# Performance work log

Measured on AMD Instinct MI355X. Metric: run time of the kernel, lower is better.

## Reference

```python
import jax, jax.numpy as jnp
import numpy as np

MAX_LANES = 5
DELTA_V = 1.0
DELTA_D = 6.0


def setup_inputs() -> dict:
    key = jax.random.key(0)
    k1, k2 = jax.random.split(key)
    targets = jax.random.randint(k1, (32, 360, 640), 0, 6, dtype=jnp.int32)
    embedding_vector = jax.random.normal(k2, (32, 4, 360, 640), dtype=jnp.float32)
    return {"targets": targets, "embedding_vector": embedding_vector}


def reference(targets, embedding_vector):
    B, C, H, W = embedding_vector.shape
    L = MAX_LANES
    P = H * W
    t = targets.reshape(B, P)                      # [B,P] labels 0..L
    e = embedding_vector.reshape(B, C, P)          # [B,C,P]

    # per-(batch, lane) segment counts and means
    onehot = (t[:, None, :] == jnp.arange(1, L + 1, dtype=t.dtype)[None, :, None])  # [B,L,P]
    counts = onehot.sum(-1)                        # [B,L] int
    valid = counts > 1                             # lane used only if >1 points
    sums = jnp.einsum('blp,bcp->blc', onehot.astype(e.dtype), e)   # [B,L,C]
    means = sums / jnp.maximum(counts, 1)[..., None].astype(e.dtype)  # [B,L,C]

    # ---- variance (pull) loss: per-point distance to its lane mean ----
    means_ext = jnp.concatenate([jnp.zeros((B, 1, C), e.dtype), means], axis=1)  # [B,L+1,C]
    mean_pix = jnp.take_along_axis(means_ext, t[..., None].astype(jnp.int32), axis=1)  # [B,P,C]
    diff = e.transpose(0, 2, 1) - mean_pix         # [B,P,C]
    sq = jnp.sum(diff * diff, axis=-1)             # [B,P]
    dist = jnp.sqrt(jnp.maximum(sq, 1e-12))
    valid_ext = jnp.concatenate([jnp.zeros((B, 1), bool), valid], axis=1)  # [B,L+1]
    pix_valid = jnp.take_along_axis(valid_ext, t.astype(jnp.int32), axis=1)  # [B,P]
    hinge = jax.nn.relu(dist - DELTA_V)
    dist_sum = jnp.sum(jnp.where(pix_valid, hinge * hinge, 0.0))
    point_count = jnp.sum(jnp.where(valid, counts, 0)).astype(e.dtype)
    dist_loss = jnp.where(point_count > 0, dist_sum / jnp.maximum(point_count, 1.0), 0.0)

    # ---- distance (push) loss: pdist over valid lane means per batch ----
    d = means[:, :, None, :] - means[:, None, :, :]          # [B,L,L,C]
    psq = jnp.sum(d * d, axis=-1)                            # [B,L,L]
    pd = jnp.sqrt(jnp.maximum(psq, 1e-12))
    iu = jnp.arange(L)
    pair_mask = valid[:, :, None] & valid[:, None, :] & (iu[:, None] < iu[None, :])  # [B,L,L]
    ph = jax.nn.relu(DELTA_D - pd)
    per_batch_sum = jnp.sum(jnp.where(pair_mask, ph * ph, 0.0), axis=(1, 2))  # [B]
    npairs = pair_mask.sum((1, 2)).astype(e.dtype)           # [B]
    batch_has = npairs > 0                                   # needs >=2 valid lanes
    var_b = jnp.where(batch_has, per_batch_sum / jnp.maximum(npairs, 1.0), 0.0)
    n_batches = batch_has.sum().astype(e.dtype)
    var_loss = jnp.where(n_batches > 0, var_b.sum() / jnp.maximum(n_batches, 1.0), 0.0)

    return dist_loss + var_loss
```

## Files before the change

### kernel.cpp

```cpp
#include <hip/hip_runtime.h>
#include <math.h>

#define B 32
#define C 4
#define H 360
#define W 640
#define P (H*W)
#define L 5
#define DELTA_V 1.0f
#define DELTA_D 6.0f

#define NV 25
#define BLK1 32
#define NBLK (B*BLK1)
#define G4 (P/4)

__device__ __forceinline__ float waveReduce(float v) {
#pragma unroll
    for (int off = 32; off; off >>= 1) v += __shfl_down(v, off, 64);
    return v;
}

__global__ __launch_bounds__(256) void seg_sums_k(const int* __restrict__ tgt,
                                                  const float* __restrict__ emb,
                                                  float* __restrict__ part1) {
    const int b = blockIdx.y;
    float s[L][C];
    float cn[L];
#pragma unroll
    for (int l = 0; l < L; ++l) {
        cn[l] = 0.f;
#pragma unroll
        for (int c = 0; c < C; ++c) s[l][c] = 0.f;
    }

    const int4*   t4 = (const int4*)(tgt + (size_t)b * P);
    const float4* e0 = (const float4*)(emb + (size_t)(b*C + 0) * P);
    const float4* e1 = (const float4*)(emb + (size_t)(b*C + 1) * P);
    const float4* e2 = (const float4*)(emb + (size_t)(b*C + 2) * P);
    const float4* e3 = (const float4*)(emb + (size_t)(b*C + 3) * P);

    auto proc = [&](int tt, float x0, float x1, float x2, float x3) {
#pragma unroll
        for (int l = 0; l < L; ++l) {
            float m = (tt == l + 1) ? 1.0f : 0.0f;
            cn[l] += m;
            s[l][0] = fmaf(m, x0, s[l][0]);
            s[l][1] = fmaf(m, x1, s[l][1]);
            s[l][2] = fmaf(m, x2, s[l][2]);
            s[l][3] = fmaf(m, x3, s[l][3]);
        }
    };

    for (int g = blockIdx.x * 256 + threadIdx.x; g < G4; g += BLK1 * 256) {
        int4   t  = t4[g];
        float4 a0 = e0[g], a1 = e1[g], a2 = e2[g], a3 = e3[g];
        proc(t.x, a0.x, a1.x, a2.x, a3.x);
        proc(t.y, a0.y, a1.y, a2.y, a3.y);
        proc(t.z, a0.z, a1.z, a2.z, a3.z);
        proc(t.w, a0.w, a1.w, a2.w, a3.w);
    }

    float vals[NV];
#pragma unroll
    for (int l = 0; l < L; ++l) {
#pragma unroll
        for (int c = 0; c < C; ++c) vals[l*4 + c] = s[l][c];
        vals[20 + l] = cn[l];
    }

    __shared__ float red[4][NV];
    const int lane = threadIdx.x & 63, wave = threadIdx.x >> 6;
#pragma unroll
    for (int k = 0; k < NV; ++k) {
        float r = waveReduce(vals[k]);
        if (lane == 0) red[wave][k] = r;
    }
    __syncthreads();
    if (threadIdx.x < NV) {
        float r = red[0][threadIdx.x] + red[1][threadIdx.x]
                + red[2][threadIdx.x] + red[3][threadIdx.x];
        part1[(size_t)(b * BLK1 + blockIdx.x) * NV + threadIdx.x] = r;
    }
}

__global__ __launch_bounds__(256) void finalize_k(const float* __restrict__ part1,
                                                  float* __restrict__ means,
                                                  float* __restrict__ validf,
                                                  float* __restrict__ misc) {
    __shared__ float smean[B*L*C];
    __shared__ float svalid[B*L];
    __shared__ float lred[4];
    const int tid = threadIdx.x;
    const int lane = tid & 63, wave = tid >> 6;

    float pc = 0.f;
    if (tid < B*L) {
        const int b = tid / L, l = tid % L;
        float sm[C] = {0.f, 0.f, 0.f, 0.f};
        float cnt = 0.f;
        for (int blk = 0; blk < BLK1; ++blk) {
            const float* p = part1 + (size_t)(b * BLK1 + blk) * NV;
#pragma unroll
            for (int c = 0; c < C; ++c) sm[c] += p[l*4 + c];
            cnt += p[20 + l];
        }
        const float inv = 1.0f / fmaxf(cnt, 1.0f);
        const bool  v   = cnt > 1.5f;
#pragma unroll
        for (int c = 0; c < C; ++c) {
            float m = sm[c] * inv;
            smean[tid*C + c] = m;
            means[tid*C + c] = m;
        }
        svalid[tid] = v ? 1.f : 0.f;
        validf[tid] = v ? 1.f : 0.f;
        if (v) pc = cnt;
    }

    {
        float r = waveReduce(pc);
        if (lane == 0) lred[wave] = r;
    }
    __syncthreads();
    if (tid == 0) misc[1] = lred[0] + lred[1] + lred[2] + lred[3];

    float vb = 0.f, has = 0.f;
    if (tid < B) {
        const int base = tid * L;
        float ssum = 0.f, np = 0.f;
#pragma unroll
        for (int i = 0; i < L; ++i) {
#pragma unroll
            for (int j = i + 1; j < L; ++j) {
                float ok = svalid[base+i] * svalid[base+j];
                float d0 = smean[(base+i)*C+0] - smean[(base+j)*C+0];
                float d1 = smean[(base+i)*C+1] - smean[(base+j)*C+1];
                float d2 = smean[(base+i)*C+2] - smean[(base+j)*C+2];
                float d3 = smean[(base+i)*C+3] - smean[(base+j)*C+3];
                float psq = d0*d0 + d1*d1 + d2*d2 + d3*d3;
                float pd  = sqrtf(fmaxf(psq, 1e-12f));
                float ph  = fmaxf(DELTA_D - pd, 0.f);
                ssum += ok * ph * ph;
                np   += ok;
            }
        }
        if (np > 0.f) { vb = ssum / np; has = 1.f; }
    }
    if (wave == 0) {
        float vr = waveReduce(vb);
        float hr = waveReduce(has);
        if (tid == 0) misc[0] = (hr > 0.f) ? vr / hr : 0.f;
    }
}

__global__ __launch_bounds__(256) void pull_k(const int* __restrict__ tgt,
                                              const float* __restrict__ emb,
                                              const float* __restrict__ means,
                                              const float* __restrict__ validf,
                                              float* __restrict__ part3) {
    __shared__ float4 lmean[L + 1];
    __shared__ float  lvalid[L + 1];
    __shared__ float  lred[4];
    const int b = blockIdx.y;
    const int tid = threadIdx.x;

    if (tid == 0) { lmean[0] = make_float4(0.f, 0.f, 0.f, 0.f); lvalid[0] = 0.f; }
    else if (tid <= L) {
        lmean[tid]  = *(const float4*)(means + ((size_t)b*L + (tid-1)) * C);
        lvalid[tid] = validf[b*L + (tid-1)];
    }
    __syncthreads();

    const int4*   t4 = (const int4*)(tgt + (size_t)b * P);
    const float4* e0 = (const float4*)(emb + (size_t)(b*C + 0) * P);
    const float4* e1 = (const float4*)(emb + (size_t)(b*C + 1) * P);
    const float4* e2 = (const float4*)(emb + (size_t)(b*C + 2) * P);
    const float4* e3 = (const float4*)(emb + (size_t)(b*C + 3) * P);

    float acc = 0.f;
    auto proc = [&](int tt, float x0, float x1, float x2, float x3) {
        float4 m = lmean[tt];
        float d0 = x0 - m.x, d1 = x1 - m.y, d2 = x2 - m.z, d3 = x3 - m.w;
        float sq   = d0*d0 + d1*d1 + d2*d2 + d3*d3;
        float dist = sqrtf(fmaxf(sq, 1e-12f));
        float h    = fmaxf(dist - DELTA_V, 0.f);
        acc = fmaf(lvalid[tt] * h, h, acc);
    };

    for (int g = blockIdx.x * 256 + threadIdx.x; g < G4; g += BLK1 * 256) {
        int4   t  = t4[g];
        float4 a0 = e0[g], a1 = e1[g], a2 = e2[g], a3 = e3[g];
        proc(t.x, a0.x, a1.x, a2.x, a3.x);
        proc(t.y, a0.y, a1.y, a2.y, a3.y);
        proc(t.z, a0.z, a1.z, a2.z, a3.z);
        proc(t.w, a0.w, a1.w, a2.w, a3.w);
    }

    float r = waveReduce(acc);
    const int lane = tid & 63, wave = tid >> 6;
    if (lane == 0) lred[wave] = r;
    __syncthreads();
    if (tid == 0)
        part3[b * BLK1 + blockIdx.x] = lred[0] + lred[1] + lred[2] + lred[3];
}

__global__ __launch_bounds__(256) void finish_k(const float* __restrict__ part3,
                                                const float* __restrict__ misc,
                                                float* __restrict__ out) {
    __shared__ float lred[4];
    const int tid = threadIdx.x;
    float s = 0.f;
    for (int i = tid; i < NBLK; i += 256) s += part3[i];
    float r = waveReduce(s);
    const int lane = tid & 63, wave = tid >> 6;
    if (lane == 0) lred[wave] = r;
    __syncthreads();
    if (tid == 0) {
        float ds  = lred[0] + lred[1] + lred[2] + lred[3];
        float pcv = misc[1];
        float dl  = (pcv > 0.f) ? ds / fmaxf(pcv, 1.0f) : 0.f;
        out[0] = dl + misc[0];
    }
}

extern "C" void kernel_launch(void* const* d_in, const int* in_sizes, int n_in,
                              void* d_out, int out_size, void* d_ws, size_t ws_size,
                              hipStream_t stream) {
    const int*   tgt = (const int*)d_in[0];
    const float* emb = (const float*)d_in[1];

    float* ws     = (float*)d_ws;
    float* part1  = ws;
    float* means  = part1 + (size_t)NBLK * NV;
    float* validf = means + B*L*C;
    float* misc   = validf + B*L;
    float* part3  = misc + 4;

    dim3 grid(BLK1, B);
    seg_sums_k<<<grid, 256, 0, stream>>>(tgt, emb, part1);
    finalize_k<<<1, 256, 0, stream>>>(part1, means, validf, misc);
    pull_k<<<grid, 256, 0, stream>>>(tgt, emb, means, validf, part3);
    finish_k<<<1, 256, 0, stream>>>(part3, misc, (float*)d_out);
}
```

Baseline: 227.4 us.

## Fuse all four loss kernels into one cooperative persistent kernel with grid syncs

Replaces the four launches with a single cooperative kernel that computes segment sums, lane means, the pull loss and the final reduction, separated by grid-wide syncs. Work is split into 2048 fixed tiles spread over a persistent grid sized from occupancy, and the inner loop is unrolled two float4 groups per iteration. The means finalisation is now spread across blocks instead of running on a single block. This removes launch gaps and the serial single-block finalize, at the cost of grid-sync overhead and a hardcoded 256-CU grid assumption.

```diff
diff --git a/kernel.cpp b/kernel.cpp
--- a/kernel.cpp
+++ b/kernel.cpp
@@ -1,19 +1,20 @@
 #include <hip/hip_runtime.h>
+#include <hip/hip_cooperative_groups.h>
 #include <math.h>
 
+namespace cg = cooperative_groups;
+
 #define B 32
-#define C 4
-#define H 360
-#define W 640
-#define P (H*W)
+#define P (360*640)
 #define L 5
 #define DELTA_V 1.0f
 #define DELTA_D 6.0f
 
-#define NV 25
-#define BLK1 32
-#define NBLK (B*BLK1)
 #define G4 (P/4)
+#define CHUNKS 64
+#define NT (B*CHUNKS)
+#define CG 900
+#define NVP 32
 
 __device__ __forceinline__ float waveReduce(float v) {
 #pragma unroll
@@ -21,206 +22,197 @@
     return v;
 }
 
-__global__ __launch_bounds__(256) void seg_sums_k(const int* __restrict__ tgt,
+__global__ __launch_bounds__(256, 4) void fused_k(const int* __restrict__ tgt,
                                                   const float* __restrict__ emb,
-                                                  float* __restrict__ part1) {
-    const int b = blockIdx.y;
-    float s[L][C];
-    float cn[L];
-#pragma unroll
-    for (int l = 0; l < L; ++l) {
-        cn[l] = 0.f;
-#pragma unroll
-        for (int c = 0; c < C; ++c) s[l][c] = 0.f;
-    }
-
-    const int4*   t4 = (const int4*)(tgt + (size_t)b * P);
-    const float4* e0 = (const float4*)(emb + (size_t)(b*C + 0) * P);
-    const float4* e1 = (const float4*)(emb + (size_t)(b*C + 1) * P);
-    const float4* e2 = (const float4*)(emb + (size_t)(b*C + 2) * P);
-    const float4* e3 = (const float4*)(emb + (size_t)(b*C + 3) * P);
-
-    auto proc = [&](int tt, float x0, float x1, float x2, float x3) {
+                                                  float* ws, float* out) {
+    cg::grid_group gg = cg::this_grid();
+    const int tid  = threadIdx.x;
+    const int lane = tid & 63, wave = tid >> 6;
+    const int nb   = gridDim.x;
+
+    float* part   = ws;
+    float* means  = part + (size_t)NT*NVP;
+    float* validf = means + B*L*4;
+    float* cntv   = validf + B*L;
+    float* pullp  = cntv + B*L;
+
+    __shared__ float  red[4][32];
+    __shared__ float4 lmean[8];
+    __shared__ float  lvalid[8];
+
+    for (int tile = blockIdx.x; tile < NT; tile += nb) {
+        const int b  = tile >> 6;
+        const int gs = (tile & 63) * CG, ge = gs + CG;
+        const int4*   t4 = (const int4*)(tgt + (size_t)b * P);
+        const float4* e0 = (const float4*)(emb + (size_t)(b*4+0) * P);
+        const float4* e1 = (const float4*)(emb + (size_t)(b*4+1) * P);
+        const float4* e2 = (const float4*)(emb + (size_t)(b*4+2) * P);
+        const float4* e3 = (const float4*)(emb + (size_t)(b*4+3) * P);
+
+        float s[L][4], cn[L];
+#pragma unroll
+        for (int l = 0; l < L; ++l) { cn[l]=0.f; s[l][0]=s[l][1]=s[l][2]=s[l][3]=0.f; }
+
+        auto proc = [&](int tt, float x0, float x1, float x2, float x3) {
+#pragma unroll
+            for (int l = 0; l < L; ++l) {
+                float m = (tt == l+1) ? 1.f : 0.f;
+                cn[l] += m;
+                s[l][0] = fmaf(m, x0, s[l][0]);
+                s[l][1] = fmaf(m, x1, s[l][1]);
+                s[l][2] = fmaf(m, x2, s[l][2]);
+                s[l][3] = fmaf(m, x3, s[l][3]);
+            }
+        };
+
+        for (int g0 = gs + tid; g0 < ge; g0 += 512) {
+            const int g1  = g0 + 256;
+            const int gg1 = (g1 < ge) ? g1 : g0;
+            int4   t0v = t4[g0],  t1v = t4[gg1];
+            float4 a00 = e0[g0],  a01 = e1[g0],  a02 = e2[g0],  a03 = e3[g0];
+            float4 a10 = e0[gg1], a11 = e1[gg1], a12 = e2[gg1], a13 = e3[gg1];
+            if (g1 >= ge) { t1v.x = 0; t1v.y = 0; t1v.z = 0; t1v.w = 0; }
+            proc(t0v.x, a00.x, a01.x, a02.x, a03.x);
+            proc(t0v.y, a00.y, a01.y, a02.y, a03.y);
+            proc(t0v.z, a00.z, a01.z, a02.z, a03.z);
+            proc(t0v.w, a00.w, a01.w, a02.w, a03.w);
+            proc(t1v.x, a10.x, a11.x, a12.x, a13.x);
+            proc(t1v.y, a10.y, a11.y, a12.y, a13.y);
+            proc(t1v.z, a10.z, a11.z, a12.z, a13.z);
+            proc(t1v.w, a10.w, a11.w, a12.w, a13.w);
+        }
+
+        float vals[25];
 #pragma unroll
         for (int l = 0; l < L; ++l) {
-            float m = (tt == l + 1) ? 1.0f : 0.0f;
-            cn[l] += m;
-            s[l][0] = fmaf(m, x0, s[l][0]);
-            s[l][1] = fmaf(m, x1, s[l][1]);
-            s[l][2] = fmaf(m, x2, s[l][2]);
-            s[l][3] = fmaf(m, x3, s[l][3]);
-        }
-    };
-
-    for (int g = blockIdx.x * 256 + threadIdx.x; g < G4; g += BLK1 * 256) {
-        int4   t  = t4[g];
-        float4 a0 = e0[g], a1 = e1[g], a2 = e2[g], a3 = e3[g];
-        proc(t.x, a0.x, a1.x, a2.x, a3.x);
-        proc(t.y, a0.y, a1.y, a2.y, a3.y);
-        proc(t.z, a0.z, a1.z, a2.z, a3.z);
-        proc(t.w, a0.w, a1.w, a2.w, a3.w);
-    }
-
-    float vals[NV];
-#pragma unroll
-    for (int l = 0; l < L; ++l) {
-#pragma unroll
-        for (int c = 0; c < C; ++c) vals[l*4 + c] = s[l][c];
-        vals[20 + l] = cn[l];
-    }
-
-    __shared__ float red[4][NV];
-    const int lane = threadIdx.x & 63, wave = threadIdx.x >> 6;
-#pragma unroll
-    for (int k = 0; k < NV; ++k) {
-        float r = waveReduce(vals[k]);
-        if (lane == 0) red[wave][k] = r;
-    }
-    __syncthreads();
-    if (threadIdx.x < NV) {
-        float r = red[0][threadIdx.x] + red[1][threadIdx.x]
-                + red[2][threadIdx.x] + red[3][threadIdx.x];
-        part1[(size_t)(b * BLK1 + blockIdx.x) * NV + threadIdx.x] = r;
-    }
-}
-
-__global__ __launch_bounds__(256) void finalize_k(const float* __restrict__ part1,
-                                                  float* __restrict__ means,
-                                                  float* __restrict__ validf,
-                                                  float* __restrict__ misc) {
-    __shared__ float smean[B*L*C];
-    __shared__ float svalid[B*L];
-    __shared__ float lred[4];
-    const int tid = threadIdx.x;
-    const int lane = tid & 63, wave = tid >> 6;
-
-    float pc = 0.f;
-    if (tid < B*L) {
-        const int b = tid / L, l = tid % L;
-        float sm[C] = {0.f, 0.f, 0.f, 0.f};
-        float cnt = 0.f;
-        for (int blk = 0; blk < BLK1; ++blk) {
-            const float* p = part1 + (size_t)(b * BLK1 + blk) * NV;
-#pragma unroll
-            for (int c = 0; c < C; ++c) sm[c] += p[l*4 + c];
-            cnt += p[20 + l];
-        }
-        const float inv = 1.0f / fmaxf(cnt, 1.0f);
-        const bool  v   = cnt > 1.5f;
-#pragma unroll
-        for (int c = 0; c < C; ++c) {
-            float m = sm[c] * inv;
-            smean[tid*C + c] = m;
-            means[tid*C + c] = m;
-        }
-        svalid[tid] = v ? 1.f : 0.f;
-        validf[tid] = v ? 1.f : 0.f;
-        if (v) pc = cnt;
-    }
-
-    {
-        float r = waveReduce(pc);
-        if (lane == 0) lred[wave] = r;
-    }
-    __syncthreads();
-    if (tid == 0) misc[1] = lred[0] + lred[1] + lred[2] + lred[3];
+            vals[l*4+0]=s[l][0]; vals[l*4+1]=s[l][1];
+            vals[l*4+2]=s[l][2]; vals[l*4+3]=s[l][3];
+            vals[20+l]=cn[l];
+        }
+#pragma unroll
+        for (int k = 0; k < 25; ++k) {
+            float r = waveReduce(vals[k]);
+            if (lane == 0) red[wave][k] = r;
+        }
+        __syncthreads();
+        if (tid < 25)
+            part[(size_t)tile*NVP + tid] = red[0][tid]+red[1][tid]+red[2][tid]+red[3][tid];
+        __syncthreads();
+    }
+    gg.sync();
+
+    for (int sg = blockIdx.x; sg < B*L; sg += nb) {
+        if (tid < 64) {
+            const int bb = sg / L, l = sg % L;
+            const float* pp = part + (size_t)(bb*CHUNKS + tid) * NVP;
+            float v0=pp[l*4+0], v1=pp[l*4+1], v2=pp[l*4+2], v3=pp[l*4+3], vc=pp[20+l];
+            v0=waveReduce(v0); v1=waveReduce(v1); v2=waveReduce(v2);
+            v3=waveReduce(v3); vc=waveReduce(vc);
+            if (lane == 0) {
+                const float inv = 1.f / fmaxf(vc, 1.f);
+                const bool  vl  = vc > 1.5f;
+                means[sg*4+0]=v0*inv; means[sg*4+1]=v1*inv;
+                means[sg*4+2]=v2*inv; means[sg*4+3]=v3*inv;
+                validf[sg] = vl ? 1.f : 0.f;
+                cntv[sg]   = vl ? vc  : 0.f;
+            }
+        }
+    }
+    gg.sync();
+
+    for (int tile = blockIdx.x; tile < NT; tile += nb) {
+        const int b  = tile >> 6;
+        const int gs = (tile & 63) * CG, ge = gs + CG;
+        __syncthreads();
+        if (tid == 0) { lmean[0] = make_float4(0.f,0.f,0.f,0.f); lvalid[0] = 0.f; }
+        else if (tid <= L) {
+            lmean[tid]  = *(const float4*)(means + ((size_t)b*L + tid-1)*4);
+            lvalid[tid] = validf[b*L + tid-1];
+        }
+        __syncthreads();
+
+        const int4*   t4 = (const int4*)(tgt + (size_t)b * P);
+        const float4* e0 = (const float4*)(emb + (size_t)(b*4+0) * P);
+        const float4* e1 = (const float4*)(emb + (size_t)(b*4+1) * P);
+        const float4* e2 = (const float4*)(emb + (size_t)(b*4+2) * P);
+        const float4* e3 = (const float4*)(emb + (size_t)(b*4+3) * P);
+
+        float acc = 0.f;
+        auto proc3 = [&](int tt, float x0, float x1, float x2, float x3) {
+            float4 m = lmean[tt];
+            float d0 = x0-m.x, d1 = x1-m.y, d2 = x2-m.z, d3 = x3-m.w;
+            float sq   = d0*d0 + d1*d1 + d2*d2 + d3*d3;
+            float dist = sqrtf(fmaxf(sq, 1e-12f));
+            float h    = fmaxf(dist - DELTA_V, 0.f);
+            acc = fmaf(lvalid[tt]*h, h, acc);
+        };
+
+        for (int g0 = gs + tid; g0 < ge; g0 += 512) {
+            const int g1  = g0 + 256;
+            const int gg1 = (g1 < ge) ? g1 : g0;
+            int4   t0v = t4[g0],  t1v = t4[gg1];
+            float4 a00 = e0[g0],  a01 = e1[g0],  a02 = e2[g0],  a03 = e3[g0];
+            float4 a10 = e0[gg1], a11 = e1[gg1], a12 = e2[gg1], a13 = e3[gg1];
+            if (g1 >= ge) { t1v.x = 0; t1v.y = 0; t1v.z = 0; t1v.w = 0; }
+            proc3(t0v.x, a00.x, a01.x, a02.x, a03.x);
+            proc3(t0v.y, a00.y, a01.y, a02.y, a03.y);
+            proc3(t0v.z, a00.z, a01.z, a02.z, a03.z);
+            proc3(t0v.w, a00.w, a01.w, a02.w, a03.w);
+            proc3(t1v.x, a10.x, a11.x, a12.x, a13.x);
+            proc3(t1v.y, a10.y, a11.y, a12.y, a13.y);
+            proc3(t1v.z, a10.z, a11.z, a12.z, a13.z);
+            proc3(t1v.w, a10.w, a11.w, a12.w, a13.w);
+        }
+
+        float r = waveReduce(acc);
+        if (lane == 0) red[wave][0] = r;
+        __syncthreads();
+        if (tid == 0) pullp[tile] = red[0][0]+red[1][0]+red[2][0]+red[3][0];
+    }
+    gg.sync();
+
+    if (blockIdx.x != 0) return;
 
     float vb = 0.f, has = 0.f;
     if (tid < B) {
-        const int base = tid * L;
+        const float* mb = means  + tid*L*4;
+        const float* vv = validf + tid*L;
         float ssum = 0.f, np = 0.f;
 #pragma unroll
-        for (int i = 0; i < L; ++i) {
-#pragma unroll
-            for (int j = i + 1; j < L; ++j) {
-                float ok = svalid[base+i] * svalid[base+j];
-                float d0 = smean[(base+i)*C+0] - smean[(base+j)*C+0];
-                float d1 = smean[(base+i)*C+1] - smean[(base+j)*C+1];
-                float d2 = smean[(base+i)*C+2] - smean[(base+j)*C+2];
-                float d3 = smean[(base+i)*C+3] - smean[(base+j)*C+3];
+        for (int i = 0; i < L; ++i)
+#pragma unroll
+            for (int j = i+1; j < L; ++j) {
+                float ok = vv[i]*vv[j];
+                float d0 = mb[i*4+0]-mb[j*4+0];
+                float d1 = mb[i*4+1]-mb[j*4+1];
+                float d2 = mb[i*4+2]-mb[j*4+2];
+                float d3 = mb[i*4+3]-mb[j*4+3];
                 float psq = d0*d0 + d1*d1 + d2*d2 + d3*d3;
                 float pd  = sqrtf(fmaxf(psq, 1e-12f));
                 float ph  = fmaxf(DELTA_D - pd, 0.f);
-                ssum += ok * ph * ph;
+                ssum += ok*ph*ph;
                 np   += ok;
             }
-        }
-        if (np > 0.f) { vb = ssum / np; has = 1.f; }
-    }
-    if (wave == 0) {
-        float vr = waveReduce(vb);
-        float hr = waveReduce(has);
-        if (tid == 0) misc[0] = (hr > 0.f) ? vr / hr : 0.f;
-    }
-}
-
-__global__ __launch_bounds__(256) void pull_k(const int* __restrict__ tgt,
-                                              const float* __restrict__ emb,
-                                              const float* __restrict__ means,
-                                              const float* __restrict__ validf,
-                                              float* __restrict__ part3) {
-    __shared__ float4 lmean[L + 1];
-    __shared__ float  lvalid[L + 1];
-    __shared__ float  lred[4];
-    const int b = blockIdx.y;
-    const int tid = threadIdx.x;
-
-    if (tid == 0) { lmean[0] = make_float4(0.f, 0.f, 0.f, 0.f); lvalid[0] = 0.f; }
-    else if (tid <= L) {
-        lmean[tid]  = *(const float4*)(means + ((size_t)b*L + (tid-1)) * C);
-        lvalid[tid] = validf[b*L + (tid-1)];
-    }
-    __syncthreads();
-
-    const int4*   t4 = (const int4*)(tgt + (size_t)b * P);
-    const float4* e0 = (const float4*)(emb + (size_t)(b*C + 0) * P);
-    const float4* e1 = (const float4*)(emb + (size_t)(b*C + 1) * P);
-    const float4* e2 = (const float4*)(emb + (size_t)(b*C + 2) * P);
-    const float4* e3 = (const float4*)(emb + (size_t)(b*C + 3) * P);
-
-    float acc = 0.f;
-    auto proc = [&](int tt, float x0, float x1, float x2, float x3) {
-        float4 m = lmean[tt];
-        float d0 = x0 - m.x, d1 = x1 - m.y, d2 = x2 - m.z, d3 = x3 - m.w;
-        float sq   = d0*d0 + d1*d1 + d2*d2 + d3*d3;
-        float dist = sqrtf(fmaxf(sq, 1e-12f));
-        float h    = fmaxf(dist - DELTA_V, 0.f);
-        acc = fmaf(lvalid[tt] * h, h, acc);
-    };
-
-    for (int g = blockIdx.x * 256 + threadIdx.x; g < G4; g += BLK1 * 256) {
-        int4   t  = t4[g];
-        float4 a0 = e0[g], a1 = e1[g], a2 = e2[g], a3 = e3[g];
-        proc(t.x, a0.x, a1.x, a2.x, a3.x);
-        proc(t.y, a0.y, a1.y, a2.y, a3.y);
-        proc(t.z, a0.z, a1.z, a2.z, a3.z);
-        proc(t.w, a0.w, a1.w, a2.w, a3.w);
-    }
-
-    float r = waveReduce(acc);
-    const int lane = tid & 63, wave = tid >> 6;
-    if (lane == 0) lred[wave] = r;
-    __syncthreads();
-    if (tid == 0)
-        part3[b * BLK1 + blockIdx.x] = lred[0] + lred[1] + lred[2] + lred[3];
-}
-
-__global__ __launch_bounds__(256) void finish_k(const float* __restrict__ part3,
-                                                const float* __restrict__ misc,
-                                                float* __restrict__ out) {
-    __shared__ float lred[4];
-    const int tid = threadIdx.x;
-    float s = 0.f;
-    for (int i = tid; i < NBLK; i += 256) s += part3[i];
-    float r = waveReduce(s);
-    const int lane = tid & 63, wave = tid >> 6;
-    if (lane == 0) lred[wave] = r;
+        if (np > 0.f) { vb = ssum/np; has = 1.f; }
+    }
+    float pc = (tid < B*L) ? cntv[tid] : 0.f;
+    float ps = 0.f;
+    for (int i = tid; i < NT; i += 256) ps += pullp[i];
+
+    float rvb = waveReduce(vb);
+    float rhs = waveReduce(has);
+    float rpc = waveReduce(pc);
+    float rps = waveReduce(ps);
+    if (lane == 0) { red[wave][0]=rvb; red[wave][1]=rhs; red[wave][2]=rpc; red[wave][3]=rps; }
     __syncthreads();
     if (tid == 0) {
-        float ds  = lred[0] + lred[1] + lred[2] + lred[3];
-        float pcv = misc[1];
-        float dl  = (pcv > 0.f) ? ds / fmaxf(pcv, 1.0f) : 0.f;
-        out[0] = dl + misc[0];
+        float svb = red[0][0]+red[1][0]+red[2][0]+red[3][0];
+        float shs = red[0][1]+red[1][1]+red[2][1]+red[3][1];
+        float spc = red[0][2]+red[1][2]+red[2][2]+red[3][2];
+        float sps = red[0][3]+red[1][3]+red[2][3]+red[3][3];
+        float var = (shs > 0.f) ? svb/shs : 0.f;
+        float dl  = (spc > 0.f) ? sps/fmaxf(spc, 1.f) : 0.f;
+        out[0] = dl + var;
     }
 }
 
@@ -229,17 +221,16 @@
                               hipStream_t stream) {
     const int*   tgt = (const int*)d_in[0];
     const float* emb = (const float*)d_in[1];
-
-    float* ws     = (float*)d_ws;
-    float* part1  = ws;
-    float* means  = part1 + (size_t)NBLK * NV;
-    float* validf = means + B*L*C;
-    float* misc   = validf + B*L;
-    float* part3  = misc + 4;
-
-    dim3 grid(BLK1, B);
-    seg_sums_k<<<grid, 256, 0, stream>>>(tgt, emb, part1);
-    finalize_k<<<1, 256, 0, stream>>>(part1, means, validf, misc);
-    pull_k<<<grid, 256, 0, stream>>>(tgt, emb, means, validf, part3);
-    finish_k<<<1, 256, 0, stream>>>(part3, misc, (float*)d_out);
+    float* ws  = (float*)d_ws;
+    float* out = (float*)d_out;
+
+    int maxB = 4;
+    (void)hipOccupancyMaxActiveBlocksPerMultiprocessor(&maxB, fused_k, 256, 0);
+    if (maxB < 1) maxB = 1;
+    int grid = maxB * 256;
+    if (grid > NT) grid = NT;
+
+    void* args[] = {(void*)&tgt, (void*)&emb, (void*)&ws, (void*)&out};
+    (void)hipLaunchCooperativeKernel((void*)fused_k, dim3(grid), dim3(256),
+                                     args, 0, stream);
 }
```

New measurement: 408.5 us. 79.7% more time.
